# Kernel tuning notes

Hardware: AMD Instinct MI355X
Metric: run time of the kernel (lower is better)

Reference implementation:

```python
import jax, jax.numpy as jnp
import numpy as np

GROUPS = 8
EPS = 1e-5


def setup_inputs() -> dict:
    key = jax.random.key(0)
    ks = jax.random.split(key, 3)
    b, c, h, w = 8, 256, 64, 64
    return {
        "x": jax.random.normal(ks[0], (b, c, h, w), dtype=jnp.float32),
        "norm_w": jnp.ones((c,), jnp.float32),
        "norm_b": jnp.zeros((c,), jnp.float32),
        "qkv_w": jax.random.normal(ks[1], (3 * c, c), dtype=jnp.float32) * (1.0 / np.sqrt(c)),
        "qkv_b": jnp.zeros((3 * c,), jnp.float32),
        "proj_w": jax.random.normal(ks[2], (c, c), dtype=jnp.float32) * (1.0 / np.sqrt(c)),
        "proj_b": jnp.zeros((c,), jnp.float32),
    }


def _group_norm(x, w, b):
    B, C, H, W = x.shape
    xg = x.reshape(B, GROUPS, C // GROUPS, H, W)
    mean = xg.mean(axis=(2, 3, 4), keepdims=True)
    var = xg.var(axis=(2, 3, 4), keepdims=True)
    xn = ((xg - mean) * jax.lax.rsqrt(var + EPS)).reshape(B, C, H, W)
    return xn * w[None, :, None, None] + b[None, :, None, None]


def reference(x, norm_w, norm_b, qkv_w, qkv_b, proj_w, proj_b):
    B, C, H, W = x.shape
    xn = _group_norm(x, norm_w, norm_b)
    # 1x1 conv == per-pixel matmul: [B,3C,H,W]
    qkv = jnp.einsum('bchw,oc->bohw', xn, qkv_w) + qkv_b[None, :, None, None]
    q, k, v = jnp.split(qkv, 3, axis=1)  # each [B,C,H,W]
    hw = H * W
    q = q.reshape(B, C, hw).transpose(0, 2, 1)  # [B,hw,C]
    k = k.reshape(B, C, hw)                     # [B,C,hw]
    v = v.reshape(B, C, hw).transpose(0, 2, 1)  # [B,hw,C]
    scores = jnp.einsum('bnc,bcm->bnm', q, k) / jnp.sqrt(jnp.asarray(C, x.dtype))
    attn = jax.nn.softmax(scores, axis=-1)      # [B,hw,hw]
    out = jnp.einsum('bnm,bmc->bnc', attn, v)   # [B,hw,C]
    out = out.transpose(0, 2, 1).reshape(B, C, H, W)
    out = jnp.einsum('bchw,oc->bohw', out, proj_w) + proj_b[None, :, None, None]
    return x + out
```

## Files before the change

### kernel.cpp

```cpp
#include <hip/hip_runtime.h>
#include <stdint.h>

#define BATCH 8
#define CH 256
#define HW 4096
#define OC 768

typedef __bf16 bf16;
typedef __attribute__((ext_vector_type(8))) __bf16 bf16x8;
typedef __attribute__((ext_vector_type(4))) __bf16 bf16x4;
typedef __attribute__((ext_vector_type(4))) float f32x4;
typedef __attribute__((ext_vector_type(4))) int i32x4;
typedef __attribute__((ext_vector_type(8))) int i32x8;
typedef long fp8x8;

#define MFMA16(a, b, c) __builtin_amdgcn_mfma_f32_16x16x32_bf16(a, b, c, 0, 0, 0)
#define MFMA8(a, b, c) __builtin_amdgcn_mfma_f32_16x16x32_fp8_fp8(a, b, c, 0, 0, 0)
#define MFMA_MX(a, b, c) __builtin_amdgcn_mfma_scale_f32_16x16x128_f8f6f4( \
    a, b, c, 0, 0, 0, 0x7F7F7F7F, 0, 0x7F7F7F7F)
#define LOG2E 1.44269504088896f

static __device__ __forceinline__ void gl2lds16(const void* g, void* l) {
  __builtin_amdgcn_global_load_lds((const __attribute__((address_space(1))) void*)g,
                                   (__attribute__((address_space(3))) void*)l, 16, 0, 0);
}

static __device__ __forceinline__ int pack4fp8(float a, float b, float c, float d) {
  int t = __builtin_amdgcn_cvt_pk_fp8_f32(a, b, 0, false);
  return __builtin_amdgcn_cvt_pk_fp8_f32(c, d, t, true);
}

__global__ __launch_bounds__(256) void trans_stats(const float* __restrict__ x,
    bf16* __restrict__ xt, float* __restrict__ partial) {
  __shared__ float tile[32][33];
  __shared__ float red[8];
  int b = blockIdx.z, ct = blockIdx.y, pt = blockIdx.x;
  int p0 = pt * 32, c0 = ct * 32;
  const float* xb = x + (size_t)b * CH * HW;
  float s = 0.f, s2 = 0.f;
#pragma unroll
  for (int i = 0; i < 4; i++) {
    int c = c0 + threadIdx.y + i * 8;
    float v = xb[(size_t)c * HW + p0 + threadIdx.x];
    tile[threadIdx.y + i * 8][threadIdx.x] = v;
    s += v;
    s2 += v * v;
  }
  int tid = threadIdx.y * 32 + threadIdx.x;
  for (int off = 32; off; off >>= 1) { s += __shfl_down(s, off); s2 += __shfl_down(s2, off); }
  if ((tid & 63) == 0) { red[(tid >> 6) * 2] = s; red[(tid >> 6) * 2 + 1] = s2; }
  __syncthreads();
  if (tid == 0) {
    float* pp = partial + ((size_t)(b * 8 + ct) * 128 + pt) * 2;
    pp[0] = red[0] + red[2] + red[4] + red[6];
    pp[1] = red[1] + red[3] + red[5] + red[7];
  }
  bf16* xtb = xt + (size_t)b * HW * CH;
#pragma unroll
  for (int i = 0; i < 4; i++) {
    int p = p0 + threadIdx.y + i * 8;
    xtb[(size_t)p * CH + c0 + threadIdx.x] = (bf16)tile[threadIdx.x][threadIdx.y + i * 8];
  }
}

__global__ __launch_bounds__(128) void gn_finalize(const float* __restrict__ partial,
    const float* __restrict__ nw, const float* __restrict__ nb,
    float* __restrict__ scale, float* __restrict__ shift) {
  int bg = blockIdx.x;
  int t = threadIdx.x;
  const float* pp = partial + (size_t)bg * 128 * 2;
  float s = pp[t * 2], s2 = pp[t * 2 + 1];
  __shared__ float red[4], mm[2];
  for (int off = 32; off; off >>= 1) { s += __shfl_down(s, off); s2 += __shfl_down(s2, off); }
  if ((t & 63) == 0) { red[(t >> 6) * 2] = s; red[(t >> 6) * 2 + 1] = s2; }
  __syncthreads();
  if (t == 0) {
    float ts = red[0] + red[2], ts2 = red[1] + red[3];
    float mean = ts * (1.0f / 131072.0f);
    float var = ts2 * (1.0f / 131072.0f) - mean * mean;
    mm[0] = mean;
    mm[1] = rsqrtf(var + 1e-5f);
  }
  __syncthreads();
  if (t < 32) {
    int b = bg >> 3, g = bg & 7, c = g * 32 + t;
    float sc = nw[c] * mm[1];
    scale[b * CH + c] = sc;
    shift[b * CH + c] = nb[c] - mm[0] * sc;
  }
}

__global__ __launch_bounds__(256) void fold_qkv(const float* __restrict__ qkv_w,
    const float* __restrict__ qkv_b, const float* __restrict__ scale,
    const float* __restrict__ shift, bf16* __restrict__ wq, float* __restrict__ bq) {
  int o = blockIdx.x, b = blockIdx.y, c = threadIdx.x;
  float w = qkv_w[o * CH + c];
  wq[((size_t)b * OC + o) * CH + c] = (bf16)(w * scale[b * CH + c]);
  float part = w * shift[b * CH + c];
  __shared__ float red[4];
  for (int off = 32; off; off >>= 1) part += __shfl_down(part, off);
  if ((threadIdx.x & 63) == 0) red[threadIdx.x >> 6] = part;
  __syncthreads();
  if (threadIdx.x == 0) bq[b * OC + o] = qkv_b[o] + red[0] + red[1] + red[2] + red[3];
}

__global__ __launch_bounds__(256) void conv_projw(const float* __restrict__ w,
                                                  bf16* __restrict__ wb) {
  int i = blockIdx.x * 256 + threadIdx.x;
  wb[i] = (bf16)w[i];
}

__global__ __launch_bounds__(256) void qkv_gemm(const bf16* __restrict__ wq,
    const float* __restrict__ bq, const bf16* __restrict__ xt,
    uint8_t* __restrict__ qt, uint8_t* __restrict__ kt, uint8_t* __restrict__ vv) {
  __shared__ __align__(16) bf16 As[2][128 * 32];
  __shared__ __align__(16) bf16 Bs[2][128 * 32];
  int b = blockIdx.z, row0 = blockIdx.y * 128, col0 = blockIdx.x * 128;
  const bf16* A = wq + (size_t)b * OC * CH + (size_t)row0 * CH;
  const bf16* Bt = xt + (size_t)b * HW * CH + (size_t)col0 * CH;
  int tid = threadIdx.x, lane = tid & 63, wave = tid >> 6;
  int wm = (wave & 1) * 64, wn = (wave >> 1) * 64;
  int l15 = lane & 15, quad = lane >> 4;
  auto stage = [&](int buf, int k0) {
#pragma unroll
    for (int i = 0; i < 2; i++) {
      int idx = i * 256 + tid, r = idx >> 2, ch = idx & 3;
      gl2lds16(A + (size_t)r * CH + k0 + ch * 8, &As[buf][idx * 8]);
    }
#pragma unroll
    for (int i = 0; i < 2; i++) {
      int idx = i * 256 + tid, r = idx >> 2, ch = idx & 3;
      gl2lds16(Bt + (size_t)r * CH + k0 + ch * 8, &Bs[buf][idx * 8]);
    }
  };
  f32x4 zero = {0.f, 0.f, 0.f, 0.f};
  f32x4 acc[4][4];
#pragma unroll
  for (int i = 0; i < 4; i++)
#pragma unroll
    for (int j = 0; j < 4; j++) acc[i][j] = zero;
  stage(0, 0);
  for (int kk = 0; kk < 8; kk++) {
    int cur = kk & 1;
    __syncthreads();
    if (kk < 7) stage(1 - cur, (kk + 1) * 32);
    bf16x8 af[4], bfr[4];
#pragma unroll
    for (int i = 0; i < 4; i++) {
      af[i] = *(const bf16x8*)(&As[cur][(wm + i * 16 + l15) * 32 + quad * 8]);
      bfr[i] = *(const bf16x8*)(&Bs[cur][(wn + i * 16 + l15) * 32 + quad * 8]);
    }
#pragma unroll
    for (int i = 0; i < 4; i++)
#pragma unroll
      for (int j = 0; j < 4; j++) acc[i][j] = MFMA16(af[i], bfr[j], acc[i][j]);
  }
  __syncthreads();
  uint8_t* tb = (uint8_t*)&As[0][0];
  int y = blockIdx.y;
  if (y < 4) {
    float sc = (y < 2) ? LOG2E : 1.0f;
#pragma unroll
    for (int i = 0; i < 4; i++) {
      int o_l = wm + i * 16 + quad * 4;
#pragma unroll
      for (int j = 0; j < 4; j++) {
        int p_l = wn + j * 16 + l15;
        float v[4];
#pragma unroll
        for (int r = 0; r < 4; r++) v[r] = (acc[i][j][r] + bq[b * OC + row0 + o_l + r]) * sc;
        *(int*)(tb + p_l * 128 + (o_l ^ ((p_l & 7) << 4))) =
            pack4fp8(v[0], v[1], v[2], v[3]);
      }
    }
    __syncthreads();
    uint8_t* dst = (y < 2) ? (qt + (size_t)b * HW * CH + row0)
                           : (kt + (size_t)b * HW * CH + (row0 - 256));
#pragma unroll
    for (int ii = 0; ii < 4; ii++) {
      int idx = ii * 256 + tid, p_l = idx >> 3, k = idx & 7;
      i32x4 d = *(const i32x4*)(tb + p_l * 128 + ((k * 16) ^ ((p_l & 7) << 4)));
      *(i32x4*)(dst + (size_t)(col0 + p_l) * CH + k * 16) = d;
    }
  } else {
#pragma unroll
    for (int i = 0; i < 4; i++) {
      int o_l = wm + i * 16 + quad * 4;
      int swz = ((o_l >> 2) & 7) << 4;
#pragma unroll
      for (int j = 0; j < 4; j++) {
        int p_l = wn + j * 16 + l15;
#pragma unroll
        for (int r = 0; r < 4; r++) {
          float vf = acc[i][j][r] + bq[b * OC + row0 + o_l + r];
          int t8 = __builtin_amdgcn_cvt_pk_fp8_f32(vf, 0.f, 0, false);
          tb[(o_l + r) * 128 + (p_l ^ swz)] = (uint8_t)(t8 & 0xff);
        }
      }
    }
    __syncthreads();
    uint8_t* dst = vv + ((size_t)b * CH + (row0 - 512)) * HW + col0;
#pragma unroll
    for (int ii = 0; ii < 4; ii++) {
      int idx = ii * 256 + tid, c_l = idx >> 3, k = idx & 7;
      i32x4 d = *(const i32x4*)(tb + c_l * 128 + ((k * 16) ^ (((c_l >> 2) & 7) << 4)));
      *(i32x4*)(dst + (size_t)c_l * HW + k * 16) = d;
    }
  }
}

__global__ __launch_bounds__(256, 2) void attn(const uint8_t* __restrict__ qt,
    const uint8_t* __restrict__ kt, const uint8_t* __restrict__ vv,
    bf16* __restrict__ opart, float* __restrict__ lstat) {
  __shared__ __align__(16) uint8_t Ks[2][32 * 256];
  __shared__ __align__(16) uint8_t Vs[3][256 * 32];
  int lin = blockIdx.x + 32 * (blockIdx.y + 2 * blockIdx.z);
  int pair = (lin & 7) * 2 + ((lin >> 3) & 1);
  int b = pair >> 1, mh = pair & 1, q0 = (lin >> 4) * 128;
  int tid = threadIdx.x, lane = tid & 63, w = tid >> 6;
  int l15 = lane & 15, quad = lane >> 4;
  int q1 = quad >> 1, qh = quad & 1;
  const uint8_t* kb_base = kt + (size_t)b * HW * CH;
  const uint8_t* vb_base = vv + (size_t)b * CH * HW;
  auto stageK = [&](int buf, int m0) {
    const uint8_t* kb = kb_base + (size_t)m0 * CH;
#pragma unroll
    for (int i = 0; i < 2; i++) {
      int idx = i * 256 + tid, m = idx >> 4, p16 = idx & 15;
      gl2lds16(kb + m * CH + (p16 ^ (m & 7)) * 16, &Ks[buf][idx * 16]);
    }
  };
  auto stageV = [&](int buf, int m0) {
#pragma unroll
    for (int i = 0; i < 2; i++) {
      int idx = i * 256 + tid, c = idx >> 1;
      int h2 = (idx & 1) ^ ((idx >> 3) & 1);
      gl2lds16(vb_base + (size_t)c * HW + m0 + h2 * 16, &Vs[buf][idx * 16]);
    }
  };
  i32x8 qf[2][2];
  const uint8_t* qb = qt + ((size_t)b * HW + q0 + w * 32) * CH;
#pragma unroll
  for (int ns = 0; ns < 2; ns++)
#pragma unroll
    for (int kc = 0; kc < 2; kc++) {
      const uint8_t* p = qb + (size_t)(ns * 16 + l15) * CH + kc * 128 + quad * 32;
      i32x4 lo = *(const i32x4*)p;
      i32x4 hi = *(const i32x4*)(p + 16);
      i32x8 q8 = {lo[0], lo[1], lo[2], lo[3], hi[0], hi[1], hi[2], hi[3]};
      qf[ns][kc] = q8;
    }
  f32x4 zero = {0.f, 0.f, 0.f, 0.f};
  f32x4 o[2][16];
#pragma unroll
  for (int ns = 0; ns < 2; ns++)
#pragma unroll
    for (int t = 0; t < 16; t++) o[ns][t] = zero;
  float lsum[2] = {0.f, 0.f};
  int kswz = l15 & 7;
  int vswz = (l15 >> 2) & 1;

  auto qk = [&](int kbuf, f32x4 (&s)[2][2]) {
#pragma unroll
    for (int kc = 0; kc < 2; kc++) {
#pragma unroll
      for (int ms = 0; ms < 2; ms++) {
        const uint8_t* base = &Ks[kbuf][(ms * 16 + l15) * 256];
        i32x4 lo = *(const i32x4*)(base + (((kc * 8 + quad * 2 + 0) ^ kswz) * 16));
        i32x4 hi = *(const i32x4*)(base + (((kc * 8 + quad * 2 + 1) ^ kswz) * 16));
        i32x8 kf = {lo[0], lo[1], lo[2], lo[3], hi[0], hi[1], hi[2], hi[3]};
#pragma unroll
        for (int ns = 0; ns < 2; ns++) s[ms][ns] = MFMA_MX(kf, qf[ns][kc], s[ms][ns]);
      }
    }
  };
  auto softmax = [&](f32x4 (&s)[2][2], fp8x8 (&paOut)[2]) {
#pragma unroll
    for (int ns = 0; ns < 2; ns++) {
      float p0[4], p1[4];
#pragma unroll
      for (int r = 0; r < 4; r++) {
        p0[r] = exp2f(fmaf(s[0][ns][r], 0.0625f, -2.0f));
        lsum[ns] += p0[r];
      }
#pragma unroll
      for (int r = 0; r < 4; r++) {
        p1[r] = exp2f(fmaf(s[1][ns][r], 0.0625f, -2.0f));
        lsum[ns] += p1[r];
      }
      int pk0 = pack4fp8(p0[0], p0[1], p0[2], p0[3]);
      int pk1 = pack4fp8(p1[0], p1[1], p1[2], p1[3]);
      int srcLo = ((quad & 1) * 32 + l15) << 2;
      int srcHi = srcLo + 64;
      int a0 = __builtin_amdgcn_ds_bpermute(srcLo, pk0);
      int a1 = __builtin_amdgcn_ds_bpermute(srcLo, pk1);
      int b0 = __builtin_amdgcn_ds_bpermute(srcHi, pk0);
      int b1 = __builtin_amdgcn_ds_bpermute(srcHi, pk1);
      int2 pr;
      pr.x = q1 ? a1 : a0;
      pr.y = q1 ? b1 : b0;
      paOut[ns] = __builtin_bit_cast(long, pr);
    }
  };
  auto pv_half = [&](int vbuf, fp8x8 (&pa)[2], int t0) {
#pragma unroll
    for (int t8 = 0; t8 < 8; t8++) {
      int t = t0 + t8;
      fp8x8 vf = *(const fp8x8*)(&Vs[vbuf][(2 * (t * 16 + l15) + (q1 ^ vswz)) * 16 + qh * 8]);
      o[0][t] = MFMA8(vf, pa[0], o[0][t]);
      o[1][t] = MFMA8(vf, pa[1], o[1][t]);
    }
  };

  int m0base = mh * 2048;
  int vread = 0;
  int vstage = 2;
  stageK(0, m0base);
  stageV(0, m0base);
  stageK(1, m0base + 32);
  stageV(1, m0base + 32);
  __syncthreads();
  fp8x8 paA[2], paB[2];
  {
    f32x4 s[2][2] = {{zero, zero}, {zero, zero}};
    qk(0, s);
    softmax(s, paA);
  }
  auto body = [&](int i, fp8x8 (&paPrev)[2], fp8x8 (&paCur)[2]) {
    int kcur = i & 1;
    __syncthreads();
    if (i < 63) {
      int m0n = m0base + (i + 1) * 32;
      stageK(1 - kcur, m0n);
      stageV(vstage, m0n);
      vstage = (vstage == 2) ? 0 : vstage + 1;
    }
    f32x4 s[2][2] = {{zero, zero}, {zero, zero}};
    __builtin_amdgcn_s_setprio(1);
    qk(kcur, s);
    pv_half(vread, paPrev, 0);
    softmax(s, paCur);
    pv_half(vread, paPrev, 8);
    __builtin_amdgcn_s_setprio(0);
    vread = (vread == 2) ? 0 : vread + 1;
  };
  for (int ii = 1; ii <= 61; ii += 2) {
    body(ii, paA, paB);
    body(ii + 1, paB, paA);
  }
  body(63, paA, paB);
  pv_half(vread, paB, 0);
  pv_half(vread, paB, 8);
  int ncol = q0 + w * 32 + l15;
#pragma unroll
  for (int ns = 0; ns < 2; ns++) {
    float lt = lsum[ns];
    lt += __shfl_xor(lt, 16);
    lt += __shfl_xor(lt, 32);
    float inv = 1.0f / lt;
    bf16* ob = opart + (size_t)(mh * BATCH + b) * CH * HW + ncol + ns * 16;
#pragma unroll
    for (int t = 0; t < 16; t++)
#pragma unroll
      for (int r = 0; r < 4; r++)
        ob[(size_t)(t * 16 + quad * 4 + r) * HW] = (bf16)(o[ns][t][r] * inv);
    if (quad == 0)
      lstat[(size_t)(mh * BATCH + b) * HW + ncol + ns * 16] = lt;
  }
}

__global__ __launch_bounds__(256) void combine_t(const bf16* __restrict__ opart,
    const float* __restrict__ lstat, bf16* __restrict__ ot) {
  __shared__ float tile[32][33];
  int b = blockIdx.z, p0 = blockIdx.x * 32, c0 = blockIdx.y * 32;
  int tx = threadIdx.x, ty = threadIdx.y;
  int p = p0 + tx;
  float l0 = lstat[(size_t)(0 * BATCH + b) * HW + p];
  float l1 = lstat[(size_t)(1 * BATCH + b) * HW + p];
  float inv = 1.0f / (l0 + l1);
  float w0 = l0 * inv, w1 = l1 * inv;
#pragma unroll
  for (int i = 0; i < 4; i++) {
    int c = c0 + ty + i * 8;
    tile[ty + i * 8][tx] =
        w0 * (float)opart[((size_t)(0 * BATCH + b) * CH + c) * HW + p] +
        w1 * (float)opart[((size_t)(1 * BATCH + b) * CH + c) * HW + p];
  }
  __syncthreads();
#pragma unroll
  for (int i = 0; i < 4; i++) {
    int pp = p0 + ty + i * 8;
    ot[((size_t)b * HW + pp) * CH + c0 + tx] = (bf16)tile[tx][ty + i * 8];
  }
}

__global__ __launch_bounds__(256) void proj_gemm(const bf16* __restrict__ pw,
    const float* __restrict__ pbias, const bf16* __restrict__ ot,
    const float* __restrict__ x, float* __restrict__ out) {
  __shared__ __align__(16) bf16 As[2][128 * 32];
  __shared__ __align__(16) bf16 Bs[2][128 * 32];
  int b = blockIdx.z, row0 = blockIdx.y * 128, col0 = blockIdx.x * 128;
  const bf16* A = pw + (size_t)row0 * CH;
  const bf16* Bt = ot + (size_t)b * HW * CH + (size_t)col0 * CH;
  int tid = threadIdx.x, lane = tid & 63, wave = tid >> 6;
  int wm = (wave & 1) * 64, wn = (wave >> 1) * 64;
  int l15 = lane & 15, quad = lane >> 4;
  auto stage = [&](int buf, int k0) {
#pragma unroll
    for (int i = 0; i < 2; i++) {
      int idx = i * 256 + tid, r = idx >> 2, ch = idx & 3;
      gl2lds16(A + (size_t)r * CH + k0 + ch * 8, &As[buf][idx * 8]);
    }
#pragma unroll
    for (int i = 0; i < 2; i++) {
      int idx = i * 256 + tid, r = idx >> 2, ch = idx & 3;
      gl2lds16(Bt + (size_t)r * CH + k0 + ch * 8, &Bs[buf][idx * 8]);
    }
  };
  f32x4 zero = {0.f, 0.f, 0.f, 0.f};
  f32x4 acc[4][4];
#pragma unroll
  for (int i = 0; i < 4; i++)
#pragma unroll
    for (int j = 0; j < 4; j++) acc[i][j] = zero;
  stage(0, 0);
  for (int kk = 0; kk < 8; kk++) {
    int cur = kk & 1;
    __syncthreads();
    if (kk < 7) stage(1 - cur, (kk + 1) * 32);
    bf16x8 af[4], bfr[4];
#pragma unroll
    for (int i = 0; i < 4; i++) {
      af[i] = *(const bf16x8*)(&As[cur][(wm + i * 16 + l15) * 32 + quad * 8]);
      bfr[i] = *(const bf16x8*)(&Bs[cur][(wn + i * 16 + l15) * 32 + quad * 8]);
    }
#pragma unroll
    for (int i = 0; i < 4; i++)
#pragma unroll
      for (int j = 0; j < 4; j++) acc[i][j] = MFMA16(af[i], bfr[j], acc[i][j]);
  }
#pragma unroll
  for (int i = 0; i < 4; i++) {
#pragma unroll
    for (int j = 0; j < 4; j++) {
      int p = col0 + wn + j * 16 + l15;
#pragma unroll
      for (int r = 0; r < 4; r++) {
        int oo = row0 + wm + i * 16 + quad * 4 + r;
        size_t off = ((size_t)b * CH + oo) * HW + p;
        out[off] = x[off] + pbias[oo] + acc[i][j][r];
      }
    }
  }
}

extern "C" void kernel_launch(void* const* d_in, const int* in_sizes, int n_in,
                              void* d_out, int out_size, void* d_ws, size_t ws_size,
                              hipStream_t stream) {
  const float* x = (const float*)d_in[0];
  const float* nw = (const float*)d_in[1];
  const float* nb = (const float*)d_in[2];
  const float* qkvw = (const float*)d_in[3];
  const float* qkvb = (const float*)d_in[4];
  const float* projw = (const float*)d_in[5];
  const float* projb = (const float*)d_in[6];
  float* out = (float*)d_out;
  char* ws = (char*)d_ws;
  float* scale = (float*)(ws + 0);
  float* shift = (float*)(ws + 8192);
  float* bq    = (float*)(ws + 16384);
  bf16* pwb    = (bf16*)(ws + 40960);
  bf16* wq     = (bf16*)(ws + 172032);
  bf16* xt     = (bf16*)(ws + 3317760);
  uint8_t* qt  = (uint8_t*)(ws + 20094976);
  uint8_t* kt  = (uint8_t*)(ws + 36872192);
  uint8_t* vv  = (uint8_t*)(ws + 53649408);
  bf16* opart  = (bf16*)(ws + 70426624);
  float* lstat = (float*)(ws + 103981056);
  float* partial = (float*)(ws + 70426624);
  bf16* ot = xt;

  trans_stats<<<dim3(128, 8, 8), dim3(32, 8), 0, stream>>>(x, xt, partial);
  gn_finalize<<<64, 128, 0, stream>>>(partial, nw, nb, scale, shift);
  fold_qkv<<<dim3(768, 8), 256, 0, stream>>>(qkvw, qkvb, scale, shift, wq, bq);
  conv_projw<<<256, 256, 0, stream>>>(projw, pwb);
  qkv_gemm<<<dim3(32, 6, 8), 256, 0, stream>>>(wq, bq, xt, qt, kt, vv);
  attn<<<dim3(32, 2, 8), 256, 0, stream>>>(qt, kt, vv, opart, lstat);
  combine_t<<<dim3(128, 8, 8), dim3(32, 8), 0, stream>>>(opart, lstat, ot);
  proj_gemm<<<dim3(32, 2, 8), 256, 0, stream>>>(pwb, projb, ot, x, out);
}
```

Baseline: 276.5 us.

## Fuse split-attention combine into projection GEMM and widen transpose-stats tiles

```diff
diff --git a/kernel.cpp b/kernel.cpp
--- a/kernel.cpp
+++ b/kernel.cpp
@@ -32,52 +32,64 @@
 
 __global__ __launch_bounds__(256) void trans_stats(const float* __restrict__ x,
     bf16* __restrict__ xt, float* __restrict__ partial) {
-  __shared__ float tile[32][33];
-  __shared__ float red[8];
+  __shared__ float tile[64][65];
+  __shared__ float red[16];
   int b = blockIdx.z, ct = blockIdx.y, pt = blockIdx.x;
-  int p0 = pt * 32, c0 = ct * 32;
+  int p0 = pt * 64, c0 = ct * 64;
+  int tid = threadIdx.x;
   const float* xb = x + (size_t)b * CH * HW;
-  float s = 0.f, s2 = 0.f;
+  float s[2] = {0.f, 0.f}, s2[2] = {0.f, 0.f};
 #pragma unroll
   for (int i = 0; i < 4; i++) {
-    int c = c0 + threadIdx.y + i * 8;
-    float v = xb[(size_t)c * HW + p0 + threadIdx.x];
-    tile[threadIdx.y + i * 8][threadIdx.x] = v;
-    s += v;
-    s2 += v * v;
-  }
-  int tid = threadIdx.y * 32 + threadIdx.x;
-  for (int off = 32; off; off >>= 1) { s += __shfl_down(s, off); s2 += __shfl_down(s2, off); }
-  if ((tid & 63) == 0) { red[(tid >> 6) * 2] = s; red[(tid >> 6) * 2 + 1] = s2; }
+    int idx = i * 256 + tid;
+    int c = idx >> 4, p4 = (idx & 15) * 4;
+    float4 v = *(const float4*)(xb + (size_t)(c0 + c) * HW + p0 + p4);
+    tile[c][p4] = v.x; tile[c][p4 + 1] = v.y; tile[c][p4 + 2] = v.z; tile[c][p4 + 3] = v.w;
+    int g = i >> 1;
+    s[g] += v.x + v.y + v.z + v.w;
+    s2[g] += v.x * v.x + v.y * v.y + v.z * v.z + v.w * v.w;
+  }
+  for (int off = 32; off; off >>= 1) {
+    s[0] += __shfl_down(s[0], off); s2[0] += __shfl_down(s2[0], off);
+    s[1] += __shfl_down(s[1], off); s2[1] += __shfl_down(s2[1], off);
+  }
+  int wv = tid >> 6;
+  if ((tid & 63) == 0) {
+    red[wv * 4 + 0] = s[0]; red[wv * 4 + 1] = s2[0];
+    red[wv * 4 + 2] = s[1]; red[wv * 4 + 3] = s2[1];
+  }
   __syncthreads();
-  if (tid == 0) {
-    float* pp = partial + ((size_t)(b * 8 + ct) * 128 + pt) * 2;
-    pp[0] = red[0] + red[2] + red[4] + red[6];
-    pp[1] = red[1] + red[3] + red[5] + red[7];
+  if (tid < 2) {
+    float ts = 0.f, ts2 = 0.f;
+#pragma unroll
+    for (int k = 0; k < 4; k++) { ts += red[k * 4 + tid * 2]; ts2 += red[k * 4 + tid * 2 + 1]; }
+    float* pp = partial + ((size_t)(b * 8 + ct * 2 + tid) * 64 + pt) * 2;
+    pp[0] = ts; pp[1] = ts2;
   }
   bf16* xtb = xt + (size_t)b * HW * CH;
 #pragma unroll
-  for (int i = 0; i < 4; i++) {
-    int p = p0 + threadIdx.y + i * 8;
-    xtb[(size_t)p * CH + c0 + threadIdx.x] = (bf16)tile[threadIdx.x][threadIdx.y + i * 8];
-  }
-}
-
-__global__ __launch_bounds__(128) void gn_finalize(const float* __restrict__ partial,
+  for (int i = 0; i < 2; i++) {
+    int idx = i * 256 + tid;
+    int p = idx >> 3, c8 = (idx & 7) * 8;
+    bf16x8 v;
+#pragma unroll
+    for (int j = 0; j < 8; j++) v[j] = (bf16)tile[c8 + j][p];
+    *(bf16x8*)(&xtb[(size_t)(p0 + p) * CH + c0 + c8]) = v;
+  }
+}
+
+__global__ __launch_bounds__(64) void gn_finalize(const float* __restrict__ partial,
     const float* __restrict__ nw, const float* __restrict__ nb,
     float* __restrict__ scale, float* __restrict__ shift) {
   int bg = blockIdx.x;
   int t = threadIdx.x;
-  const float* pp = partial + (size_t)bg * 128 * 2;
+  const float* pp = partial + (size_t)bg * 64 * 2;
   float s = pp[t * 2], s2 = pp[t * 2 + 1];
-  __shared__ float red[4], mm[2];
+  __shared__ float mm[2];
   for (int off = 32; off; off >>= 1) { s += __shfl_down(s, off); s2 += __shfl_down(s2, off); }
-  if ((t & 63) == 0) { red[(t >> 6) * 2] = s; red[(t >> 6) * 2 + 1] = s2; }
-  __syncthreads();
   if (t == 0) {
-    float ts = red[0] + red[2], ts2 = red[1] + red[3];
-    float mean = ts * (1.0f / 131072.0f);
-    float var = ts2 * (1.0f / 131072.0f) - mean * mean;
+    float mean = s * (1.0f / 131072.0f);
+    float var = s2 * (1.0f / 131072.0f) - mean * mean;
     mm[0] = mean;
     mm[1] = rsqrtf(var + 1e-5f);
   }
@@ -358,63 +370,66 @@
     lt += __shfl_xor(lt, 16);
     lt += __shfl_xor(lt, 32);
     float inv = 1.0f / lt;
-    bf16* ob = opart + (size_t)(mh * BATCH + b) * CH * HW + ncol + ns * 16;
-#pragma unroll
-    for (int t = 0; t < 16; t++)
-#pragma unroll
-      for (int r = 0; r < 4; r++)
-        ob[(size_t)(t * 16 + quad * 4 + r) * HW] = (bf16)(o[ns][t][r] * inv);
+    bf16* ob = opart + ((size_t)(mh * BATCH + b) * HW + ncol + ns * 16) * CH;
+#pragma unroll
+    for (int t = 0; t < 16; t++) {
+      bf16x4 pk;
+#pragma unroll
+      for (int r = 0; r < 4; r++) pk[r] = (bf16)(o[ns][t][r] * inv);
+      *(bf16x4*)(&ob[t * 16 + quad * 4]) = pk;
+    }
     if (quad == 0)
       lstat[(size_t)(mh * BATCH + b) * HW + ncol + ns * 16] = lt;
   }
 }
 
-__global__ __launch_bounds__(256) void combine_t(const bf16* __restrict__ opart,
-    const float* __restrict__ lstat, bf16* __restrict__ ot) {
-  __shared__ float tile[32][33];
-  int b = blockIdx.z, p0 = blockIdx.x * 32, c0 = blockIdx.y * 32;
-  int tx = threadIdx.x, ty = threadIdx.y;
-  int p = p0 + tx;
-  float l0 = lstat[(size_t)(0 * BATCH + b) * HW + p];
-  float l1 = lstat[(size_t)(1 * BATCH + b) * HW + p];
-  float inv = 1.0f / (l0 + l1);
-  float w0 = l0 * inv, w1 = l1 * inv;
-#pragma unroll
-  for (int i = 0; i < 4; i++) {
-    int c = c0 + ty + i * 8;
-    tile[ty + i * 8][tx] =
-        w0 * (float)opart[((size_t)(0 * BATCH + b) * CH + c) * HW + p] +
-        w1 * (float)opart[((size_t)(1 * BATCH + b) * CH + c) * HW + p];
-  }
-  __syncthreads();
-#pragma unroll
-  for (int i = 0; i < 4; i++) {
-    int pp = p0 + ty + i * 8;
-    ot[((size_t)b * HW + pp) * CH + c0 + tx] = (bf16)tile[tx][ty + i * 8];
-  }
-}
-
 __global__ __launch_bounds__(256) void proj_gemm(const bf16* __restrict__ pw,
-    const float* __restrict__ pbias, const bf16* __restrict__ ot,
-    const float* __restrict__ x, float* __restrict__ out) {
+    const float* __restrict__ pbias, const bf16* __restrict__ opart,
+    const float* __restrict__ lstat, const float* __restrict__ x,
+    float* __restrict__ out) {
   __shared__ __align__(16) bf16 As[2][128 * 32];
   __shared__ __align__(16) bf16 Bs[2][128 * 32];
   int b = blockIdx.z, row0 = blockIdx.y * 128, col0 = blockIdx.x * 128;
   const bf16* A = pw + (size_t)row0 * CH;
-  const bf16* Bt = ot + (size_t)b * HW * CH + (size_t)col0 * CH;
+  const bf16* op0 = opart + ((size_t)(0 * BATCH + b) * HW + col0) * CH;
+  const bf16* op1 = opart + ((size_t)(1 * BATCH + b) * HW + col0) * CH;
   int tid = threadIdx.x, lane = tid & 63, wave = tid >> 6;
   int wm = (wave & 1) * 64, wn = (wave >> 1) * 64;
   int l15 = lane & 15, quad = lane >> 4;
-  auto stage = [&](int buf, int k0) {
+  float w0a[2], w1a[2];
+#pragma unroll
+  for (int i = 0; i < 2; i++) {
+    int p = col0 + i * 64 + (tid >> 2);
+    float l0 = lstat[(size_t)(0 * BATCH + b) * HW + p];
+    float l1 = lstat[(size_t)(1 * BATCH + b) * HW + p];
+    float inv = 1.0f / (l0 + l1);
+    w0a[i] = l0 * inv;
+    w1a[i] = l1 * inv;
+  }
+  auto stageA = [&](int buf, int k0) {
 #pragma unroll
     for (int i = 0; i < 2; i++) {
       int idx = i * 256 + tid, r = idx >> 2, ch = idx & 3;
       gl2lds16(A + (size_t)r * CH + k0 + ch * 8, &As[buf][idx * 8]);
     }
-#pragma unroll
-    for (int i = 0; i < 2; i++) {
-      int idx = i * 256 + tid, r = idx >> 2, ch = idx & 3;
-      gl2lds16(Bt + (size_t)r * CH + k0 + ch * 8, &Bs[buf][idx * 8]);
+  };
+  auto loadB = [&](int k0, bf16x8 (&b0)[2], bf16x8 (&b1)[2]) {
+#pragma unroll
+    for (int i = 0; i < 2; i++) {
+      int r = i * 64 + (tid >> 2), ch = tid & 3;
+      b0[i] = *(const bf16x8*)(op0 + (size_t)r * CH + k0 + ch * 8);
+      b1[i] = *(const bf16x8*)(op1 + (size_t)r * CH + k0 + ch * 8);
+    }
+  };
+  auto writeB = [&](int buf, bf16x8 (&b0)[2], bf16x8 (&b1)[2]) {
+#pragma unroll
+    for (int i = 0; i < 2; i++) {
+      int idx = i * 256 + tid;
+      bf16x8 o8;
+#pragma unroll
+      for (int j = 0; j < 8; j++)
+        o8[j] = (bf16)(w0a[i] * (float)b0[i][j] + w1a[i] * (float)b1[i][j]);
+      *(bf16x8*)(&Bs[buf][idx * 8]) = o8;
     }
   };
   f32x4 zero = {0.f, 0.f, 0.f, 0.f};
@@ -423,11 +438,17 @@
   for (int i = 0; i < 4; i++)
 #pragma unroll
     for (int j = 0; j < 4; j++) acc[i][j] = zero;
-  stage(0, 0);
+  bf16x8 nb0[2], nb1[2];
+  stageA(0, 0);
+  loadB(0, nb0, nb1);
+  writeB(0, nb0, nb1);
   for (int kk = 0; kk < 8; kk++) {
     int cur = kk & 1;
     __syncthreads();
-    if (kk < 7) stage(1 - cur, (kk + 1) * 32);
+    if (kk < 7) {
+      stageA(1 - cur, (kk + 1) * 32);
+      loadB((kk + 1) * 32, nb0, nb1);
+    }
     bf16x8 af[4], bfr[4];
 #pragma unroll
     for (int i = 0; i < 4; i++) {
@@ -438,6 +459,7 @@
     for (int i = 0; i < 4; i++)
 #pragma unroll
       for (int j = 0; j < 4; j++) acc[i][j] = MFMA16(af[i], bfr[j], acc[i][j]);
+    if (kk < 7) writeB(1 - cur, nb0, nb1);
   }
 #pragma unroll
   for (int i = 0; i < 4; i++) {
@@ -478,14 +500,12 @@
   bf16* opart  = (bf16*)(ws + 70426624);
   float* lstat = (float*)(ws + 103981056);
   float* partial = (float*)(ws + 70426624);
-  bf16* ot = xt;
-
-  trans_stats<<<dim3(128, 8, 8), dim3(32, 8), 0, stream>>>(x, xt, partial);
-  gn_finalize<<<64, 128, 0, stream>>>(partial, nw, nb, scale, shift);
+
+  trans_stats<<<dim3(64, 4, 8), 256, 0, stream>>>(x, xt, partial);
+  gn_finalize<<<64, 64, 0, stream>>>(partial, nw, nb, scale, shift);
   fold_qkv<<<dim3(768, 8), 256, 0, stream>>>(qkvw, qkvb, scale, shift, wq, bq);
   conv_projw<<<256, 256, 0, stream>>>(projw, pwb);
   qkv_gemm<<<dim3(32, 6, 8), 256, 0, stream>>>(wq, bq, xt, qt, kt, vv);
   attn<<<dim3(32, 2, 8), 256, 0, stream>>>(qt, kt, vv, opart, lstat);
-  combine_t<<<dim3(128, 8, 8), dim3(32, 8), 0, stream>>>(opart, lstat, ot);
-  proj_gemm<<<dim3(32, 2, 8), 256, 0, stream>>>(pwb, projb, ot, x, out);
-}
+  proj_gemm<<<dim3(32, 2, 8), 256, 0, stream>>>(pwb, projb, opart, lstat, x, out);
+}
```

After: 258.4 us. -6.6%, faster.
